# Performance work log

Hardware: AMD Instinct MI355X
Metric: run time of the kernel (lower is better)

Reference implementation:

```python
import jax, jax.numpy as jnp
import numpy as np


def setup_inputs() -> dict:
    key = jax.random.key(0)
    ks = jax.random.split(key, 8)
    T, D = 8192, 36
    return {
        "embeddings": jax.random.normal(ks[0], (T, D), dtype=jnp.float32),
        "WQ_prog": jax.random.normal(ks[1], (2, D), dtype=jnp.float32),
        "WK_prog": jax.random.normal(ks[2], (2, D), dtype=jnp.float32),
        "WV_op": jax.random.normal(ks[3], (1, D), dtype=jnp.float32),
        "WV_arg": jax.random.normal(ks[4], (1, D), dtype=jnp.float32),
        "WQ_stack": jax.random.normal(ks[5], (2, D), dtype=jnp.float32),
        "WK_stack": jax.random.normal(ks[6], (2, D), dtype=jnp.float32),
        "WV_stack": jax.random.normal(ks[7], (1, D), dtype=jnp.float32),
    }


def reference(embeddings, WQ_prog, WK_prog, WV_op, WV_arg, WQ_stack, WK_stack, WV_stack):
    # --- program-fetch head: hard-argmax attention ---
    Q_prog = embeddings @ WQ_prog.T          # (T, 2)
    K_prog = embeddings @ WK_prog.T          # (T, 2)
    V_op = embeddings @ WV_op.T              # (T, 1)
    V_arg = embeddings @ WV_arg.T            # (T, 1)
    scores_prog = Q_prog @ K_prog.T          # (T, T)
    best_prog = jnp.argmax(scores_prog, axis=1)   # (T,)
    fetched_ops = V_op[best_prog, 0]
    fetched_args = V_arg[best_prog, 0]

    # --- stack-fetch head: hard-argmax attention ---
    Q_stack = embeddings @ WQ_stack.T        # (T, 2)
    K_stack = embeddings @ WK_stack.T        # (T, 2)
    V_stack = embeddings @ WV_stack.T        # (T, 1)
    scores_stack = Q_stack @ K_stack.T       # (T, T)
    best_stack = jnp.argmax(scores_stack, axis=1)
    fetched_vals = V_stack[best_stack, 0]

    return (fetched_ops, fetched_args, fetched_vals)
```

## Files before the change

### kernel.cpp

```cpp
#include <hip/hip_runtime.h>
#include <math.h>

#define T 8192
#define D 36
#define NCH 16
#define CHUNK (T / NCH)
#define RPT (CHUNK / 256)


__device__ __forceinline__ void load_row(const float* __restrict__ E, int j,
                                         float* e) {
    const float4* Er = (const float4*)(E + j * D);
#pragma unroll
    for (int i = 0; i < D / 4; ++i) {
        float4 v = Er[i];
        e[4 * i + 0] = v.x;
        e[4 * i + 1] = v.y;
        e[4 * i + 2] = v.z;
        e[4 * i + 3] = v.w;
    }
}

__global__ __launch_bounds__(256) void fused_proj_argmax(
    const float* __restrict__ E,
    const float* __restrict__ WQp, const float* __restrict__ WKp,
    const float* __restrict__ WQs, const float* __restrict__ WKs,
    float* __restrict__ pv, int* __restrict__ pi) {
    const int head = blockIdx.z;
    const float* __restrict__ WQ = head ? WQs : WQp;
    const float* __restrict__ WK = head ? WKs : WKp;

    __shared__ float2 sk[CHUNK];
    const int j0 = blockIdx.y * CHUNK;

#pragma unroll
    for (int r = 0; r < RPT; ++r) {
        const int j = j0 + r * 256 + threadIdx.x;
        float e[D];
        load_row(E, j, e);
        float k0 = 0.f, k1 = 0.f;
#pragma unroll
        for (int d = 0; d < D; ++d) {
            k0 = fmaf(e[d], WK[d], k0);
            k1 = fmaf(e[d], WK[D + d], k1);
        }
        sk[r * 256 + threadIdx.x] = make_float2(k0, k1);
    }

    const int row = blockIdx.x * 256 + threadIdx.x;
    float q0 = 0.f, q1 = 0.f;
    {
        float e[D];
        load_row(E, row, e);
#pragma unroll
        for (int d = 0; d < D; ++d) {
            q0 = fmaf(e[d], WQ[d], q0);
            q1 = fmaf(e[d], WQ[D + d], q1);
        }
    }
    __syncthreads();

    float best = -INFINITY;
    int bi = 0;
#pragma unroll 8
    for (int k = 0; k < CHUNK; ++k) {
        float2 kk = sk[k];
        float s = fmaf(q0, kk.x, q1 * kk.y);
        bool gt = s > best;
        best = gt ? s : best;
        bi = gt ? k : bi;
    }
    const int prow = head * T + row;
    pv[blockIdx.y * 2 * T + prow] = best;
    pi[blockIdx.y * 2 * T + prow] = j0 + bi;
}

__global__ __launch_bounds__(256) void finalize_fused(
    const float* __restrict__ E,
    const float* __restrict__ WVop, const float* __restrict__ WVarg,
    const float* __restrict__ WVs,
    const float* __restrict__ pv, const int* __restrict__ pi,
    float* __restrict__ out) {
    const int idx = blockIdx.x * blockDim.x + threadIdx.x;
    if (idx >= 2 * T) return;
    const int head = idx >> 13;
    const int row = idx & (T - 1);

    float best = -INFINITY;
    int bi = 0;
#pragma unroll
    for (int c = 0; c < NCH; ++c) {
        float v = pv[c * 2 * T + idx];
        int i2 = pi[c * 2 * T + idx];
        bool gt = v > best;
        best = gt ? v : best;
        bi = gt ? i2 : bi;
    }

    float e[D];
    load_row(E, bi, e);
    if (head == 0) {
        float vop = 0.f, varg = 0.f;
#pragma unroll
        for (int d = 0; d < D; ++d) {
            vop = fmaf(e[d], WVop[d], vop);
            varg = fmaf(e[d], WVarg[d], varg);
        }
        out[row] = vop;
        out[T + row] = varg;
    } else {
        float vs = 0.f;
#pragma unroll
        for (int d = 0; d < D; ++d) vs = fmaf(e[d], WVs[d], vs);
        out[2 * T + row] = vs;
    }
}

extern "C" void kernel_launch(void* const* d_in, const int* in_sizes, int n_in,
                              void* d_out, int out_size, void* d_ws,
                              size_t ws_size, hipStream_t stream) {
    const float* E = (const float*)d_in[0];
    const float* WQp = (const float*)d_in[1];
    const float* WKp = (const float*)d_in[2];
    const float* WVop = (const float*)d_in[3];
    const float* WVarg = (const float*)d_in[4];
    const float* WQs = (const float*)d_in[5];
    const float* WKs = (const float*)d_in[6];
    const float* WVs = (const float*)d_in[7];
    float* out = (float*)d_out;

    float* pv = (float*)d_ws;
    int* pi = (int*)((float*)d_ws + 2 * T * NCH);

    dim3 gA(T / 256, NCH, 2);
    fused_proj_argmax<<<gA, 256, 0, stream>>>(E, WQp, WKp, WQs, WKs, pv, pi);

    finalize_fused<<<(2 * T) / 256, 256, 0, stream>>>(E, WVop, WVarg, WVs, pv,
                                                      pi, out);
}
```

Before: 99.37 us.

## Track only max in scan, recover argmax index in wave-per-row finalize

The main scan loop now keeps only the running maximum score, processing two keys per float4 LDS load with fmaxf instead of a compare-and-select on an index. The first block column writes projected K and Q vectors to global memory. The finalize kernel uses one wave per row: it picks the winning chunk by ballot, then rescans that chunk to find the first key whose score equals the maximum. This removes index bookkeeping from the hot loop. The cost is extra global writes of Q and K and a second, partial scan per row. Exact float equality must reproduce the same score, which the shared fmaf expression is meant to guarantee.

```diff
diff --git a/kernel.cpp b/kernel.cpp
--- a/kernel.cpp
+++ b/kernel.cpp
@@ -21,11 +21,11 @@
     }
 }
 
-__global__ __launch_bounds__(256) void fused_proj_argmax(
+__global__ __launch_bounds__(256) void maxscan_kernel(
     const float* __restrict__ E,
     const float* __restrict__ WQp, const float* __restrict__ WKp,
     const float* __restrict__ WQs, const float* __restrict__ WKs,
-    float* __restrict__ pv, int* __restrict__ pi) {
+    float* __restrict__ pv, float2* __restrict__ Kg, float2* __restrict__ Qg) {
     const int head = blockIdx.z;
     const float* __restrict__ WQ = head ? WQs : WQp;
     const float* __restrict__ WK = head ? WKs : WKp;
@@ -44,7 +44,9 @@
             k0 = fmaf(e[d], WK[d], k0);
             k1 = fmaf(e[d], WK[D + d], k1);
         }
-        sk[r * 256 + threadIdx.x] = make_float2(k0, k1);
+        float2 kk = make_float2(k0, k1);
+        sk[r * 256 + threadIdx.x] = kk;
+        if (blockIdx.x == 0) Kg[head * T + j] = kk;
     }
 
     const int row = blockIdx.x * 256 + threadIdx.x;
@@ -58,43 +60,54 @@
             q1 = fmaf(e[d], WQ[D + d], q1);
         }
     }
+    if (blockIdx.y == 0) Qg[head * T + row] = make_float2(q0, q1);
     __syncthreads();
 
     float best = -INFINITY;
-    int bi = 0;
+    const float4* sk4 = (const float4*)sk;
 #pragma unroll 8
-    for (int k = 0; k < CHUNK; ++k) {
-        float2 kk = sk[k];
-        float s = fmaf(q0, kk.x, q1 * kk.y);
-        bool gt = s > best;
-        best = gt ? s : best;
-        bi = gt ? k : bi;
+    for (int k = 0; k < CHUNK / 2; ++k) {
+        float4 kk = sk4[k];
+        float s0 = fmaf(q0, kk.x, q1 * kk.y);
+        float s1 = fmaf(q0, kk.z, q1 * kk.w);
+        best = fmaxf(best, fmaxf(s0, s1));
     }
-    const int prow = head * T + row;
-    pv[blockIdx.y * 2 * T + prow] = best;
-    pi[blockIdx.y * 2 * T + prow] = j0 + bi;
+    pv[blockIdx.y * 2 * T + head * T + row] = best;
 }
 
-__global__ __launch_bounds__(256) void finalize_fused(
+__global__ __launch_bounds__(256) void finalize_wave(
     const float* __restrict__ E,
     const float* __restrict__ WVop, const float* __restrict__ WVarg,
     const float* __restrict__ WVs,
-    const float* __restrict__ pv, const int* __restrict__ pi,
-    float* __restrict__ out) {
-    const int idx = blockIdx.x * blockDim.x + threadIdx.x;
-    if (idx >= 2 * T) return;
-    const int head = idx >> 13;
-    const int row = idx & (T - 1);
+    const float* __restrict__ pv, const float2* __restrict__ Kg,
+    const float2* __restrict__ Qg, float* __restrict__ out) {
+    const int wid = threadIdx.x >> 6;
+    const int lane = threadIdx.x & 63;
+    const int prow = blockIdx.x * 4 + wid;
+    const int head = prow >> 13;
+    const int row = prow & (T - 1);
 
-    float best = -INFINITY;
+    const float v = (lane < NCH) ? pv[lane * 2 * T + prow] : -INFINITY;
+    float m = v;
+#pragma unroll
+    for (int off = 8; off; off >>= 1) m = fmaxf(m, __shfl_xor(m, off));
+    m = __shfl(m, 0);
+
+    const unsigned long long cb = __ballot(v == m);
+    const int cwin = __ffsll(cb) - 1;
+
+    const float2 q = Qg[prow];
     int bi = 0;
-#pragma unroll
-    for (int c = 0; c < NCH; ++c) {
-        float v = pv[c * 2 * T + idx];
-        int i2 = pi[c * 2 * T + idx];
-        bool gt = v > best;
-        best = gt ? v : best;
-        bi = gt ? i2 : bi;
+#pragma unroll 1
+    for (int i = 0; i < CHUNK / 64; ++i) {
+        const int j = cwin * CHUNK + i * 64 + lane;
+        const float2 kk = Kg[head * T + j];
+        const float s = fmaf(q.x, kk.x, q.y * kk.y);
+        const unsigned long long eb = __ballot(s == m);
+        if (eb) {
+            bi = cwin * CHUNK + i * 64 + __ffsll(eb) - 1;
+            break;
+        }
     }
 
     float e[D];
@@ -106,13 +119,15 @@
             vop = fmaf(e[d], WVop[d], vop);
             varg = fmaf(e[d], WVarg[d], varg);
         }
-        out[row] = vop;
-        out[T + row] = varg;
+        if (lane == 0) {
+            out[row] = vop;
+            out[T + row] = varg;
+        }
     } else {
         float vs = 0.f;
 #pragma unroll
         for (int d = 0; d < D; ++d) vs = fmaf(e[d], WVs[d], vs);
-        out[2 * T + row] = vs;
+        if (lane == 0) out[2 * T + row] = vs;
     }
 }
 
@@ -129,12 +144,14 @@
     const float* WVs = (const float*)d_in[7];
     float* out = (float*)d_out;
 
-    float* pv = (float*)d_ws;
-    int* pi = (int*)((float*)d_ws + 2 * T * NCH);
+    float* wsf = (float*)d_ws;
+    float* pv = wsf;
+    float2* Kg = (float2*)(wsf + 2 * T * NCH);
+    float2* Qg = (float2*)(wsf + 2 * T * NCH + 4 * T);
 
     dim3 gA(T / 256, NCH, 2);
-    fused_proj_argmax<<<gA, 256, 0, stream>>>(E, WQp, WKp, WQs, WKs, pv, pi);
+    maxscan_kernel<<<gA, 256, 0, stream>>>(E, WQp, WKp, WQs, WKs, pv, Kg, Qg);
 
-    finalize_fused<<<(2 * T) / 256, 256, 0, stream>>>(E, WVop, WVarg, WVs, pv,
-                                                      pi, out);
+    finalize_wave<<<(2 * T) / 4, 256, 0, stream>>>(E, WVop, WVarg, WVs, pv, Kg,
+                                                   Qg, out);
 }
```

After: 112.1 us. 12.8% more time.
